# Performance work log

Measured on AMD Instinct MI355X. Metric: run time of the kernel, lower is better.

Reference implementation:

```python
import jax, jax.numpy as jnp
import numpy as np

HIDDEN = 1024
FFN = 2048
NUM_EXPERTS = 8
TOP_K = 2
BATCH, SEQ = 2, 1024


def setup_inputs() -> dict:
    key = jax.random.key(0)
    k0, k1, k2, k3, k4 = jax.random.split(key, 5)
    scale = 0.02
    hidden_states = jax.random.normal(k0, (BATCH, SEQ, HIDDEN), dtype=jnp.float32)
    gate_w = jax.random.normal(k1, (NUM_EXPERTS, HIDDEN), dtype=jnp.float32) * scale
    w1 = jax.random.normal(k2, (NUM_EXPERTS, FFN, HIDDEN), dtype=jnp.float32) * scale  # gate proj
    w3 = jax.random.normal(k3, (NUM_EXPERTS, FFN, HIDDEN), dtype=jnp.float32) * scale  # up proj
    w2 = jax.random.normal(k4, (NUM_EXPERTS, HIDDEN, FFN), dtype=jnp.float32) * scale  # down proj
    return {"hidden_states": hidden_states, "gate_w": gate_w, "w1": w1, "w2": w2, "w3": w3}


def reference(hidden_states, gate_w, w1, w2, w3):
    B, S, D = hidden_states.shape
    x = hidden_states.reshape(-1, D)                         # [T, D]
    T = x.shape[0]
    # Router: logits -> fp32 softmax -> top-k -> renormalize
    router_logits = jnp.einsum("td,ed->te", x, gate_w)       # [T, E]
    routing_weights = jax.nn.softmax(router_logits.astype(jnp.float32), axis=1)
    top_vals, top_idx = jax.lax.top_k(routing_weights, TOP_K)  # [T, K]
    top_vals = top_vals / jnp.sum(top_vals, axis=-1, keepdims=True)
    top_vals = top_vals.astype(x.dtype)
    # Per-token-per-expert combine weight (0 for unselected experts)
    w_te = jnp.zeros((T, NUM_EXPERTS), dtype=x.dtype)
    w_te = w_te.at[jnp.arange(T)[:, None], top_idx].add(top_vals)  # [T, E]
    # Fused experts: silu(x W1^T) * (x W3^T) -> W2^T, weighted combine
    g = jax.nn.silu(jnp.einsum("td,efd->tef", x, w1))        # [T, E, F]
    u = jnp.einsum("td,efd->tef", x, w3)                     # [T, E, F]
    y = jnp.einsum("tef,edf->ted", g * u, w2)                # [T, E, D]
    out = jnp.einsum("ted,te->td", y, w_te)                  # [T, D]
    return out.reshape(B, S, D), router_logits
```

## Files before the change

kernel.cpp:

```cpp
#include <hip/hip_runtime.h>
#include <hip/hip_bf16.h>
#include <stdint.h>

#define HIDDEN  1024
#define FFN_DIM 2048
#define NEXP    8
#define NTOK    2048
#define MAXROWS 5120

typedef short bf16x8 __attribute__((ext_vector_type(8)));
typedef float f32x4  __attribute__((ext_vector_type(4)));

static const size_t OFF_CNT  = 0;
static const size_t OFF_BASE = 64;
static const size_t OFF_TOK  = 128;
static const size_t OFF_WGT  = OFF_TOK + (size_t)NEXP*NTOK*4;
static const size_t OFF_XBF  = 131328;
static const size_t XBF_B    = (size_t)NTOK*HIDDEN*2;
static const size_t OFF_H    = OFF_XBF + XBF_B;
static const size_t H_B      = (size_t)MAXROWS*FFN_DIM*2;
static const size_t WS_NEED  = OFF_H + H_B;

__device__ __forceinline__ unsigned short f2bf(float f) {
  union { float f; unsigned u; } a; a.f = f;
  unsigned r = a.u + 0x7fff + ((a.u >> 16) & 1);
  return (unsigned short)(r >> 16);
}

__device__ __forceinline__ bf16x8 cvt8b(float4 a, float4 b) {
  union { uint4 u; bf16x8 v; } r;
  asm("v_cvt_pk_bf16_f32 %0, %1, %2" : "=v"(r.u.x) : "v"(a.x), "v"(a.y));
  asm("v_cvt_pk_bf16_f32 %0, %1, %2" : "=v"(r.u.y) : "v"(a.z), "v"(a.w));
  asm("v_cvt_pk_bf16_f32 %0, %1, %2" : "=v"(r.u.z) : "v"(b.x), "v"(b.y));
  asm("v_cvt_pk_bf16_f32 %0, %1, %2" : "=v"(r.u.w) : "v"(b.z), "v"(b.w));
  return r.v;
}

__device__ __forceinline__ void ld_g2l16(const void* gsrc, void* ldst) {
  __builtin_amdgcn_global_load_lds(
      (const __attribute__((address_space(1))) unsigned int*)gsrc,
      (__attribute__((address_space(3))) unsigned int*)ldst, 16, 0, 0);
}

__global__ __launch_bounds__(256) void router_kernel(
    const float* __restrict__ x, const float* __restrict__ gw,
    float* __restrict__ logits, int* __restrict__ cnt,
    int* __restrict__ tok, float* __restrict__ wgt,
    unsigned short* __restrict__ xbf)
{
  const int t   = blockIdx.x;
  const int tid = threadIdx.x;
  float4 xv = ((const float4*)(x + (size_t)t * HIDDEN))[tid];
  if (xbf) {
    ushort4 o;
    o.x = f2bf(xv.x); o.y = f2bf(xv.y); o.z = f2bf(xv.z); o.w = f2bf(xv.w);
    ((ushort4*)(xbf + (size_t)t * HIDDEN))[tid] = o;
  }
  float p[NEXP];
#pragma unroll
  for (int e = 0; e < NEXP; ++e) {
    float4 gv = ((const float4*)(gw + (size_t)e * HIDDEN))[tid];
    p[e] = xv.x * gv.x + xv.y * gv.y + xv.z * gv.z + xv.w * gv.w;
  }
#pragma unroll
  for (int e = 0; e < NEXP; ++e) {
#pragma unroll
    for (int off = 32; off > 0; off >>= 1)
      p[e] += __shfl_down(p[e], off, 64);
  }
  __shared__ float red[4][NEXP];
  const int wv = tid >> 6, ln = tid & 63;
  if (ln == 0) {
#pragma unroll
    for (int e = 0; e < NEXP; ++e) red[wv][e] = p[e];
  }
  __syncthreads();
  if (tid == 0) {
    float l[NEXP];
#pragma unroll
    for (int e = 0; e < NEXP; ++e) {
      l[e] = red[0][e] + red[1][e] + red[2][e] + red[3][e];
      logits[(size_t)t * NEXP + e] = l[e];
    }
    int i0 = 0;
#pragma unroll
    for (int e = 1; e < NEXP; ++e) if (l[e] > l[i0]) i0 = e;
    int i1 = (i0 == 0) ? 1 : 0;
#pragma unroll
    for (int e = 0; e < NEXP; ++e) if (e != i0 && l[e] > l[i1]) i1 = e;
    float w0 = 1.f / (1.f + expf(l[i1] - l[i0]));
    float w1 = 1.f - w0;
    int s0 = atomicAdd(&cnt[i0], 1);
    tok[i0 * NTOK + s0] = t;  wgt[i0 * NTOK + s0] = w0;
    int s1 = atomicAdd(&cnt[i1], 1);
    tok[i1 * NTOK + s1] = t;  wgt[i1 * NTOK + s1] = w1;
  }
}

__global__ void prefix_kernel(const int* __restrict__ cnt, int* __restrict__ base) {
  if (threadIdx.x == 0 && blockIdx.x == 0) {
    int b = 0;
#pragma unroll
    for (int e = 0; e < NEXP; ++e) { base[e] = b; b += ((cnt[e] + 127) >> 7) << 7; }
    base[NEXP] = b;
  }
}

__global__ __launch_bounds__(256, 3) void gemm1_kernel(
    const unsigned short* __restrict__ xbf,
    const float* __restrict__ w1f,
    const float* __restrict__ w3f,
    const int* __restrict__ cnt, const int* __restrict__ base,
    const int* __restrict__ tok,
    unsigned short* __restrict__ H)
{
  const int bid  = blockIdx.x;
  const int e    = bid & 7;
  const int slot = bid >> 3;
  const int mt   = slot & 15;
  const int nt   = slot >> 4;
  const int n = cnt[e];
  if (mt * 128 >= n) return;
  const int t = threadIdx.x;
  const int w = t >> 6, l = t & 63;

  __shared__ unsigned short Xs[128 * 64];
  __shared__ float W1s[64 * 64];
  __shared__ float W3s[64 * 64];

  const int xr   = t >> 3;
  const int xkey = ((t & 7) ^ (xr & 7)) << 3;
  const unsigned short* xp[4];
#pragma unroll
  for (int c = 0; c < 4; ++c) {
    int row = min(mt * 128 + c * 32 + xr, n - 1);
    xp[c] = xbf + (size_t)tok[e * NTOK + row] * HIDDEN + xkey;
  }

  const int wr   = t >> 4;
  const int wkey = ((t & 15) ^ wr) << 2;
  const float* w1p = w1f + (size_t)e * FFN_DIM * HIDDEN + ((size_t)nt * 64 + wr) * HIDDEN + wkey;
  const float* w3p = w3f + (size_t)e * FFN_DIM * HIDDEN + ((size_t)nt * 64 + wr) * HIDDEN + wkey;

  f32x4 acc1[4][2], acc3[4][2];
#pragma unroll
  for (int i = 0; i < 4; ++i)
#pragma unroll
    for (int j = 0; j < 2; ++j) { acc1[i][j] = (f32x4)0.f; acc3[i][j] = (f32x4)0.f; }

  const int Moff = (w & 1) * 64;
  const int Noff = (w >> 1) * 32;
  const int lr = l & 15;
  const int lg = l >> 4;

  for (int kb = 0; kb < HIDDEN / 64; ++kb) {
    __syncthreads();
    const int ko = kb * 64;
#pragma unroll
    for (int c = 0; c < 4; ++c)
      ld_g2l16(xp[c] + ko, (char*)Xs + c * 4096 + w * 1024);
#pragma unroll
    for (int c = 0; c < 4; ++c) {
      ld_g2l16(w1p + (size_t)c * 16 * HIDDEN + ko, (char*)W1s + c * 4096 + w * 1024);
      ld_g2l16(w3p + (size_t)c * 16 * HIDDEN + ko, (char*)W3s + c * 4096 + w * 1024);
    }
    __syncthreads();
#pragma unroll
    for (int s = 0; s < 2; ++s) {
      const int ub = 4 * s + lg;
      bf16x8 a[4];
#pragma unroll
      for (int mi = 0; mi < 4; ++mi) {
        const int R = Moff + mi * 16 + lr;
        a[mi] = *(const bf16x8*)((const char*)Xs + R * 128 + ((ub ^ (R & 7)) << 4));
      }
#pragma unroll
      for (int ni = 0; ni < 2; ++ni) {
        const int R  = Noff + ni * 16 + lr;
        const int p0 = (2 * ub) ^ (R & 15);
        float4 lo1 = *(const float4*)((const char*)W1s + R * 256 + (p0 << 4));
        float4 hi1 = *(const float4*)((const char*)W1s + R * 256 + ((p0 ^ 1) << 4));
        float4 lo3 = *(const float4*)((const char*)W3s + R * 256 + (p0 << 4));
        float4 hi3 = *(const float4*)((const char*)W3s + R * 256 + ((p0 ^ 1) << 4));
        bf16x8 b1 = cvt8b(lo1, hi1);
        bf16x8 b3 = cvt8b(lo3, hi3);
#pragma unroll
        for (int mi = 0; mi < 4; ++mi) {
          acc1[mi][ni] = __builtin_amdgcn_mfma_f32_16x16x32_bf16(a[mi], b1, acc1[mi][ni], 0, 0, 0);
          acc3[mi][ni] = __builtin_amdgcn_mfma_f32_16x16x32_bf16(a[mi], b3, acc3[mi][ni], 0, 0, 0);
        }
      }
    }
  }

  const size_t rbase = (size_t)base[e] + (size_t)mt * 128;
#pragma unroll
  for (int mi = 0; mi < 4; ++mi)
#pragma unroll
    for (int ni = 0; ni < 2; ++ni)
#pragma unroll
      for (int j = 0; j < 4; ++j) {
        int row = Moff + mi * 16 + lg * 4 + j;
        int col = nt * 64 + Noff + ni * 16 + lr;
        float s1 = acc1[mi][ni][j], s3 = acc3[mi][ni][j];
        float h = (s1 / (1.f + __expf(-s1))) * s3;
        H[(rbase + row) * FFN_DIM + col] = f2bf(h);
      }
}

__global__ __launch_bounds__(256, 4) void gemm2_kernel(
    const unsigned short* __restrict__ H,
    const float* __restrict__ w2f,
    const int* __restrict__ cnt, const int* __restrict__ base,
    const int* __restrict__ tok, const float* __restrict__ wgt,
    float* __restrict__ out)
{
  const int bid  = blockIdx.x;
  const int e    = bid & 7;
  const int slot = bid >> 3;
  const int mt   = slot & 15;
  const int nt   = (slot >> 4) & 15;
  const int sk   = slot >> 8;
  const int n = cnt[e];
  if (mt * 128 >= n) return;
  const int t = threadIdx.x;
  const int w = t >> 6, l = t & 63;

  __shared__ unsigned short Hs[128 * 64];
  __shared__ float W2s[64 * 64];
  __shared__ int   stok[128];
  __shared__ float swgt[128];

  if (t < 128) {
    int idx = mt * 128 + t;
    int ok = idx < n;
    stok[t] = ok ? tok[e * NTOK + idx] : -1;
    swgt[t] = ok ? wgt[e * NTOK + idx] : 0.f;
  }

  const int xr   = t >> 3;
  const int xkey = ((t & 7) ^ (xr & 7)) << 3;
  const unsigned short* Hp = H + (size_t)(base[e] + mt * 128 + xr) * FFN_DIM
                               + sk * (FFN_DIM / 2) + xkey;
  const int wr   = t >> 4;
  const int wkey = ((t & 15) ^ wr) << 2;
  const float* w2p = w2f + (size_t)e * HIDDEN * FFN_DIM + ((size_t)nt * 64 + wr) * FFN_DIM
                        + sk * (FFN_DIM / 2) + wkey;

  f32x4 acc[4][2];
#pragma unroll
  for (int i = 0; i < 4; ++i)
#pragma unroll
    for (int j = 0; j < 2; ++j) acc[i][j] = (f32x4)0.f;

  const int Moff = (w & 1) * 64;
  const int Noff = (w >> 1) * 32;
  const int lr = l & 15;
  const int lg = l >> 4;

  for (int kb = 0; kb < FFN_DIM / 2 / 64; ++kb) {
    __syncthreads();
    const int ko = kb * 64;
#pragma unroll
    for (int c = 0; c < 4; ++c)
      ld_g2l16(Hp + (size_t)c * 32 * FFN_DIM + ko, (char*)Hs + c * 4096 + w * 1024);
#pragma unroll
    for (int c = 0; c < 4; ++c)
      ld_g2l16(w2p + (size_t)c * 16 * FFN_DIM + ko, (char*)W2s + c * 4096 + w * 1024);
    __syncthreads();
#pragma unroll
    for (int s = 0; s < 2; ++s) {
      const int ub = 4 * s + lg;
      bf16x8 a[4];
#pragma unroll
      for (int mi = 0; mi < 4; ++mi) {
        const int R = Moff + mi * 16 + lr;
        a[mi] = *(const bf16x8*)((const char*)Hs + R * 128 + ((ub ^ (R & 7)) << 4));
      }
#pragma unroll
      for (int ni = 0; ni < 2; ++ni) {
        const int R  = Noff + ni * 16 + lr;
        const int p0 = (2 * ub) ^ (R & 15);
        float4 lo = *(const float4*)((const char*)W2s + R * 256 + (p0 << 4));
        float4 hi = *(const float4*)((const char*)W2s + R * 256 + ((p0 ^ 1) << 4));
        bf16x8 b = cvt8b(lo, hi);
#pragma unroll
        for (int mi = 0; mi < 4; ++mi)
          acc[mi][ni] = __builtin_amdgcn_mfma_f32_16x16x32_bf16(a[mi], b, acc[mi][ni], 0, 0, 0);
      }
    }
  }

#pragma unroll
  for (int mi = 0; mi < 4; ++mi)
#pragma unroll
    for (int ni = 0; ni < 2; ++ni)
#pragma unroll
      for (int j = 0; j < 4; ++j) {
        int row = Moff + mi * 16 + lg * 4 + j;
        int tk = stok[row];
        if (tk >= 0) {
          int col = nt * 64 + Noff + ni * 16 + lr;
          atomicAdd(&out[(size_t)tk * HIDDEN + col], swgt[row] * acc[mi][ni][j]);
        }
      }
}

#define TT 12
#define FC 256
#define NCHUNK (FFN_DIM / FC)

__global__ __launch_bounds__(256) void moe_ffn_kernel(
    const float* __restrict__ x,
    const float* __restrict__ w1, const float* __restrict__ w2,
    const float* __restrict__ w3,
    const int* __restrict__ cnt, const int* __restrict__ tok,
    const float* __restrict__ wgt, float* __restrict__ out)
{
  const int e  = blockIdx.y;
  const int n  = cnt[e];
  const int ts = blockIdx.x * TT;
  if (ts >= n) return;
  const int tid = threadIdx.x;

  __shared__ float xs[TT * HIDDEN];
  __shared__ float hc[TT * FC];
  __shared__ int   stok[TT];
  __shared__ float swgt[TT];

  if (tid < TT) {
    int idx = ts + tid;
    int tk  = (idx < n) ? tok[e * NTOK + idx] : -1;
    stok[tid] = tk;
    swgt[tid] = (idx < n) ? wgt[e * NTOK + idx] : 0.f;
  }
  __syncthreads();
#pragma unroll
  for (int i = 0; i < TT; ++i) {
    int tk = stok[i];
    float4 v = make_float4(0.f, 0.f, 0.f, 0.f);
    if (tk >= 0) v = ((const float4*)(x + (size_t)tk * HIDDEN))[tid];
    ((float4*)(xs + i * HIDDEN))[tid] = v;
  }
  __syncthreads();

  const float* w1e = w1 + (size_t)e * FFN_DIM * HIDDEN;
  const float* w3e = w3 + (size_t)e * FFN_DIM * HIDDEN;
  const float* w2e = w2 + (size_t)e * HIDDEN * FFN_DIM;

  float yacc[4][TT];
#pragma unroll
  for (int j = 0; j < 4; ++j)
#pragma unroll
    for (int t = 0; t < TT; ++t) yacc[j][t] = 0.f;

  for (int c = 0; c < NCHUNK; ++c) {
    const int f = c * FC + tid;
    const float4* r1 = (const float4*)(w1e + (size_t)f * HIDDEN);
    const float4* r3 = (const float4*)(w3e + (size_t)f * HIDDEN);
    float a1[TT], a3[TT];
#pragma unroll
    for (int t = 0; t < TT; ++t) { a1[t] = 0.f; a3[t] = 0.f; }
    for (int k = 0; k < HIDDEN / 4; ++k) {
      float4 v1 = r1[k];
      float4 v3 = r3[k];
#pragma unroll
      for (int t = 0; t < TT; ++t) {
        float4 xv = *(const float4*)(xs + t * HIDDEN + 4 * k);
        a1[t] += xv.x * v1.x + xv.y * v1.y + xv.z * v1.z + xv.w * v1.w;
        a3[t] += xv.x * v3.x + xv.y * v3.y + xv.z * v3.z + xv.w * v3.w;
      }
    }
    __syncthreads();
#pragma unroll
    for (int t = 0; t < TT; ++t) {
      float g  = a1[t];
      float sg = g / (1.f + __expf(-g));
      hc[t * FC + tid] = sg * a3[t];
    }
    __syncthreads();
    const float4* r20 = (const float4*)(w2e + (size_t)(tid      ) * FFN_DIM + c * FC);
    const float4* r21 = (const float4*)(w2e + (size_t)(tid + 256) * FFN_DIM + c * FC);
    const float4* r22 = (const float4*)(w2e + (size_t)(tid + 512) * FFN_DIM + c * FC);
    const float4* r23 = (const float4*)(w2e + (size_t)(tid + 768) * FFN_DIM + c * FC);
    for (int k = 0; k < FC / 4; ++k) {
      float4 wv0 = r20[k], wv1 = r21[k], wv2 = r22[k], wv3 = r23[k];
#pragma unroll
      for (int t = 0; t < TT; ++t) {
        float4 hv = *(const float4*)(hc + t * FC + 4 * k);
        yacc[0][t] += hv.x * wv0.x + hv.y * wv0.y + hv.z * wv0.z + hv.w * wv0.w;
        yacc[1][t] += hv.x * wv1.x + hv.y * wv1.y + hv.z * wv1.z + hv.w * wv1.w;
        yacc[2][t] += hv.x * wv2.x + hv.y * wv2.y + hv.z * wv2.z + hv.w * wv2.w;
        yacc[3][t] += hv.x * wv3.x + hv.y * wv3.y + hv.z * wv3.z + hv.w * wv3.w;
      }
    }
  }

#pragma unroll
  for (int t = 0; t < TT; ++t) {
    int tk = stok[t];
    if (tk < 0) continue;
    float wt = swgt[t];
    float* orow = out + (size_t)tk * HIDDEN;
    atomicAdd(orow + tid,       wt * yacc[0][t]);
    atomicAdd(orow + tid + 256, wt * yacc[1][t]);
    atomicAdd(orow + tid + 512, wt * yacc[2][t]);
    atomicAdd(orow + tid + 768, wt * yacc[3][t]);
  }
}

extern "C" void kernel_launch(void* const* d_in, const int* in_sizes, int n_in,
                              void* d_out, int out_size, void* d_ws, size_t ws_size,
                              hipStream_t stream) {
  const float* x  = (const float*)d_in[0];
  const float* gw = (const float*)d_in[1];
  const float* w1 = (const float*)d_in[2];
  const float* w2 = (const float*)d_in[3];
  const float* w3 = (const float*)d_in[4];
  float* out    = (float*)d_out;
  float* logits = out + (size_t)NTOK * HIDDEN;

  char* ws = (char*)d_ws;
  int*   cnt  = (int*)(ws + OFF_CNT);
  int*   base = (int*)(ws + OFF_BASE);
  int*   tokp = (int*)(ws + OFF_TOK);
  float* wgtp = (float*)(ws + OFF_WGT);

  const bool big = (ws_size >= WS_NEED);
  unsigned short* xbf  = big ? (unsigned short*)(ws + OFF_XBF) : (unsigned short*)0;
  unsigned short* Hbuf = big ? (unsigned short*)(ws + OFF_H)   : (unsigned short*)0;

  hipMemsetAsync(out, 0, (size_t)NTOK * HIDDEN * sizeof(float), stream);
  hipMemsetAsync(cnt, 0, NEXP * sizeof(int), stream);

  router_kernel<<<NTOK, 256, 0, stream>>>(x, gw, logits, cnt, tokp, wgtp, xbf);

  if (big) {
    prefix_kernel<<<1, 64, 0, stream>>>(cnt, base);
    gemm1_kernel<<<NEXP * 16 * 32, 256, 0, stream>>>(xbf, w1, w3, cnt, base, tokp, Hbuf);
    gemm2_kernel<<<NEXP * 16 * 16 * 2, 256, 0, stream>>>(Hbuf, w2, cnt, base, tokp, wgtp, out);
  } else {
    dim3 grid((NTOK + TT - 1) / TT, NEXP);
    moe_ffn_kernel<<<grid, 256, 0, stream>>>(x, w1, w2, w3, cnt, tokp, wgtp, out);
  }
}
```

Before: 196.8 us.

## Double-buffer weight tiles in expert GEMMs to prefetch next k-block

Both expert GEMM kernels now keep two LDS buffers for the fp32 weight tiles and issue the next k-block's weight loads before computing on the current one. Manual vmcnt waits and raw s_barrier calls replace the two __syncthreads per iteration, so the weight fetch for the next step overlaps the MFMA work. The larger LDS footprint lowers the launch-bounds occupancy hints (3 to 2 for gemm1, 4 to 3 for gemm2), trading resident waves for latency hiding. The hand-written waitcnt counts rely on exact load-instruction counts being correct.

Result: slower. 207.7 us (+5.6%).

```diff
diff --git a/kernel.cpp b/kernel.cpp
--- a/kernel.cpp
+++ b/kernel.cpp
@@ -106,7 +106,7 @@
   }
 }
 
-__global__ __launch_bounds__(256, 3) void gemm1_kernel(
+__global__ __launch_bounds__(256, 2) void gemm1_kernel(
     const unsigned short* __restrict__ xbf,
     const float* __restrict__ w1f,
     const float* __restrict__ w3f,
@@ -125,8 +125,8 @@
   const int w = t >> 6, l = t & 63;
 
   __shared__ unsigned short Xs[128 * 64];
-  __shared__ float W1s[64 * 64];
-  __shared__ float W3s[64 * 64];
+  __shared__ float W1s[2][64 * 64];
+  __shared__ float W3s[2][64 * 64];
 
   const int xr   = t >> 3;
   const int xkey = ((t & 7) ^ (xr & 7)) << 3;
@@ -153,18 +153,32 @@
   const int lr = l & 15;
   const int lg = l >> 4;
 
+#pragma unroll
+  for (int c = 0; c < 4; ++c) {
+    ld_g2l16(w1p + (size_t)c * 16 * HIDDEN, (char*)W1s[0] + c * 4096 + w * 1024);
+    ld_g2l16(w3p + (size_t)c * 16 * HIDDEN, (char*)W3s[0] + c * 4096 + w * 1024);
+  }
+
   for (int kb = 0; kb < HIDDEN / 64; ++kb) {
-    __syncthreads();
     const int ko = kb * 64;
+    const int cb = kb & 1, nb = cb ^ 1;
 #pragma unroll
     for (int c = 0; c < 4; ++c)
       ld_g2l16(xp[c] + ko, (char*)Xs + c * 4096 + w * 1024);
-#pragma unroll
-    for (int c = 0; c < 4; ++c) {
-      ld_g2l16(w1p + (size_t)c * 16 * HIDDEN + ko, (char*)W1s + c * 4096 + w * 1024);
-      ld_g2l16(w3p + (size_t)c * 16 * HIDDEN + ko, (char*)W3s + c * 4096 + w * 1024);
-    }
-    __syncthreads();
+    if (kb < HIDDEN / 64 - 1) {
+#pragma unroll
+      for (int c = 0; c < 4; ++c) {
+        ld_g2l16(w1p + (size_t)c * 16 * HIDDEN + ko + 64, (char*)W1s[nb] + c * 4096 + w * 1024);
+        ld_g2l16(w3p + (size_t)c * 16 * HIDDEN + ko + 64, (char*)W3s[nb] + c * 4096 + w * 1024);
+      }
+      __builtin_amdgcn_sched_barrier(0);
+      asm volatile("s_waitcnt vmcnt(8)" ::: "memory");
+    } else {
+      __builtin_amdgcn_sched_barrier(0);
+      asm volatile("s_waitcnt vmcnt(0)" ::: "memory");
+    }
+    __builtin_amdgcn_s_barrier();
+    __builtin_amdgcn_sched_barrier(0);
 #pragma unroll
     for (int s = 0; s < 2; ++s) {
       const int ub = 4 * s + lg;
@@ -178,10 +192,10 @@
       for (int ni = 0; ni < 2; ++ni) {
         const int R  = Noff + ni * 16 + lr;
         const int p0 = (2 * ub) ^ (R & 15);
-        float4 lo1 = *(const float4*)((const char*)W1s + R * 256 + (p0 << 4));
-        float4 hi1 = *(const float4*)((const char*)W1s + R * 256 + ((p0 ^ 1) << 4));
-        float4 lo3 = *(const float4*)((const char*)W3s + R * 256 + (p0 << 4));
-        float4 hi3 = *(const float4*)((const char*)W3s + R * 256 + ((p0 ^ 1) << 4));
+        float4 lo1 = *(const float4*)((const char*)W1s[cb] + R * 256 + (p0 << 4));
+        float4 hi1 = *(const float4*)((const char*)W1s[cb] + R * 256 + ((p0 ^ 1) << 4));
+        float4 lo3 = *(const float4*)((const char*)W3s[cb] + R * 256 + (p0 << 4));
+        float4 hi3 = *(const float4*)((const char*)W3s[cb] + R * 256 + ((p0 ^ 1) << 4));
         bf16x8 b1 = cvt8b(lo1, hi1);
         bf16x8 b3 = cvt8b(lo3, hi3);
 #pragma unroll
@@ -191,6 +205,9 @@
         }
       }
     }
+    __builtin_amdgcn_sched_barrier(0);
+    asm volatile("s_waitcnt lgkmcnt(0)" ::: "memory");
+    __builtin_amdgcn_s_barrier();
   }
 
   const size_t rbase = (size_t)base[e] + (size_t)mt * 128;
@@ -208,7 +225,7 @@
       }
 }
 
-__global__ __launch_bounds__(256, 4) void gemm2_kernel(
+__global__ __launch_bounds__(256, 3) void gemm2_kernel(
     const unsigned short* __restrict__ H,
     const float* __restrict__ w2f,
     const int* __restrict__ cnt, const int* __restrict__ base,
@@ -227,7 +244,7 @@
   const int w = t >> 6, l = t & 63;
 
   __shared__ unsigned short Hs[128 * 64];
-  __shared__ float W2s[64 * 64];
+  __shared__ float W2s[2][64 * 64];
   __shared__ int   stok[128];
   __shared__ float swgt[128];
 
@@ -258,16 +275,28 @@
   const int lr = l & 15;
   const int lg = l >> 4;
 
+#pragma unroll
+  for (int c = 0; c < 4; ++c)
+    ld_g2l16(w2p + (size_t)c * 16 * FFN_DIM, (char*)W2s[0] + c * 4096 + w * 1024);
+
   for (int kb = 0; kb < FFN_DIM / 2 / 64; ++kb) {
-    __syncthreads();
     const int ko = kb * 64;
+    const int cb = kb & 1, nb = cb ^ 1;
 #pragma unroll
     for (int c = 0; c < 4; ++c)
       ld_g2l16(Hp + (size_t)c * 32 * FFN_DIM + ko, (char*)Hs + c * 4096 + w * 1024);
-#pragma unroll
-    for (int c = 0; c < 4; ++c)
-      ld_g2l16(w2p + (size_t)c * 16 * FFN_DIM + ko, (char*)W2s + c * 4096 + w * 1024);
-    __syncthreads();
+    if (kb < FFN_DIM / 2 / 64 - 1) {
+#pragma unroll
+      for (int c = 0; c < 4; ++c)
+        ld_g2l16(w2p + (size_t)c * 16 * FFN_DIM + ko + 64, (char*)W2s[nb] + c * 4096 + w * 1024);
+      __builtin_amdgcn_sched_barrier(0);
+      asm volatile("s_waitcnt vmcnt(4)" ::: "memory");
+    } else {
+      __builtin_amdgcn_sched_barrier(0);
+      asm volatile("s_waitcnt vmcnt(0)" ::: "memory");
+    }
+    __builtin_amdgcn_s_barrier();
+    __builtin_amdgcn_sched_barrier(0);
 #pragma unroll
     for (int s = 0; s < 2; ++s) {
       const int ub = 4 * s + lg;
@@ -281,14 +310,17 @@
       for (int ni = 0; ni < 2; ++ni) {
         const int R  = Noff + ni * 16 + lr;
         const int p0 = (2 * ub) ^ (R & 15);
-        float4 lo = *(const float4*)((const char*)W2s + R * 256 + (p0 << 4));
-        float4 hi = *(const float4*)((const char*)W2s + R * 256 + ((p0 ^ 1) << 4));
+        float4 lo = *(const float4*)((const char*)W2s[cb] + R * 256 + (p0 << 4));
+        float4 hi = *(const float4*)((const char*)W2s[cb] + R * 256 + ((p0 ^ 1) << 4));
         bf16x8 b = cvt8b(lo, hi);
 #pragma unroll
         for (int mi = 0; mi < 4; ++mi)
           acc[mi][ni] = __builtin_amdgcn_mfma_f32_16x16x32_bf16(a[mi], b, acc[mi][ni], 0, 0, 0);
       }
     }
+    __builtin_amdgcn_sched_barrier(0);
+    asm volatile("s_waitcnt lgkmcnt(0)" ::: "memory");
+    __builtin_amdgcn_s_barrier();
   }
 
 #pragma unroll
```

## Pre-convert expert weights to bf16 and retile GEMMs to 512-thread blocks

Applied to the files above, without the earlier changes.

Adds a grid-stride kernel that converts w1, w3 and w2 from fp32 to bf16 into new workspace regions on every call. Both expert GEMMs then stream bf16 weight tiles straight into LDS, dropping the per-tile fp32 LDS reads and in-loop conversions. The GEMMs also move to 512-thread blocks with 8 waves, each wave owning a 32x32 output sub-tile instead of 64x32. The trade-off is an extra full pass over all weights each call (about 192MB read, 96MB written) and a much larger workspace requirement; if the workspace is too small, the code falls back to the slow path.

Result: slower. 265.1 us (+34.7%).

```diff
diff --git a/kernel.cpp b/kernel.cpp
--- a/kernel.cpp
+++ b/kernel.cpp
@@ -17,7 +17,11 @@
 static const size_t OFF_WGT  = OFF_TOK + (size_t)NEXP*NTOK*4;
 static const size_t OFF_XBF  = 131328;
 static const size_t XBF_B    = (size_t)NTOK*HIDDEN*2;
-static const size_t OFF_H    = OFF_XBF + XBF_B;
+static const size_t OFF_W1B  = OFF_XBF + XBF_B;
+static const size_t W_B      = (size_t)NEXP*FFN_DIM*HIDDEN*2;
+static const size_t OFF_W3B  = OFF_W1B + W_B;
+static const size_t OFF_W2B  = OFF_W3B + W_B;
+static const size_t OFF_H    = OFF_W2B + W_B;
 static const size_t H_B      = (size_t)MAXROWS*FFN_DIM*2;
 static const size_t WS_NEED  = OFF_H + H_B;
 
@@ -27,13 +31,13 @@
   return (unsigned short)(r >> 16);
 }
 
-__device__ __forceinline__ bf16x8 cvt8b(float4 a, float4 b) {
-  union { uint4 u; bf16x8 v; } r;
-  asm("v_cvt_pk_bf16_f32 %0, %1, %2" : "=v"(r.u.x) : "v"(a.x), "v"(a.y));
-  asm("v_cvt_pk_bf16_f32 %0, %1, %2" : "=v"(r.u.y) : "v"(a.z), "v"(a.w));
-  asm("v_cvt_pk_bf16_f32 %0, %1, %2" : "=v"(r.u.z) : "v"(b.x), "v"(b.y));
-  asm("v_cvt_pk_bf16_f32 %0, %1, %2" : "=v"(r.u.w) : "v"(b.z), "v"(b.w));
-  return r.v;
+__device__ __forceinline__ uint4 cvt8u(float4 a, float4 b) {
+  uint4 r;
+  asm("v_cvt_pk_bf16_f32 %0, %1, %2" : "=v"(r.x) : "v"(a.x), "v"(a.y));
+  asm("v_cvt_pk_bf16_f32 %0, %1, %2" : "=v"(r.y) : "v"(a.z), "v"(a.w));
+  asm("v_cvt_pk_bf16_f32 %0, %1, %2" : "=v"(r.z) : "v"(b.x), "v"(b.y));
+  asm("v_cvt_pk_bf16_f32 %0, %1, %2" : "=v"(r.w) : "v"(b.z), "v"(b.w));
+  return r;
 }
 
 __device__ __forceinline__ void ld_g2l16(const void* gsrc, void* ldst) {
@@ -106,10 +110,29 @@
   }
 }
 
-__global__ __launch_bounds__(256, 3) void gemm1_kernel(
+__global__ __launch_bounds__(256) void cvtw_kernel(
+    const float* __restrict__ s0, const float* __restrict__ s1, const float* __restrict__ s2,
+    unsigned short* __restrict__ d0, unsigned short* __restrict__ d1, unsigned short* __restrict__ d2,
+    int n8)
+{
+  const int start  = blockIdx.x * blockDim.x + threadIdx.x;
+  const int stride = gridDim.x * blockDim.x;
+#pragma unroll
+  for (int pass = 0; pass < 3; ++pass) {
+    const float* s = (pass == 0) ? s0 : (pass == 1) ? s1 : s2;
+    unsigned short* d = (pass == 0) ? d0 : (pass == 1) ? d1 : d2;
+    for (int i = start; i < n8; i += stride) {
+      float4 a = ((const float4*)s)[2 * i];
+      float4 b = ((const float4*)s)[2 * i + 1];
+      ((uint4*)d)[i] = cvt8u(a, b);
+    }
+  }
+}
+
+__global__ __launch_bounds__(512, 6) void gemm1_kernel(
     const unsigned short* __restrict__ xbf,
-    const float* __restrict__ w1f,
-    const float* __restrict__ w3f,
+    const unsigned short* __restrict__ w1bf,
+    const unsigned short* __restrict__ w3bf,
     const int* __restrict__ cnt, const int* __restrict__ base,
     const int* __restrict__ tok,
     unsigned short* __restrict__ H)
@@ -124,78 +147,64 @@
   const int t = threadIdx.x;
   const int w = t >> 6, l = t & 63;
 
-  __shared__ unsigned short Xs[128 * 64];
-  __shared__ float W1s[64 * 64];
-  __shared__ float W3s[64 * 64];
-
-  const int xr   = t >> 3;
-  const int xkey = ((t & 7) ^ (xr & 7)) << 3;
-  const unsigned short* xp[4];
-#pragma unroll
-  for (int c = 0; c < 4; ++c) {
-    int row = min(mt * 128 + c * 32 + xr, n - 1);
-    xp[c] = xbf + (size_t)tok[e * NTOK + row] * HIDDEN + xkey;
-  }
-
-  const int wr   = t >> 4;
-  const int wkey = ((t & 15) ^ wr) << 2;
-  const float* w1p = w1f + (size_t)e * FFN_DIM * HIDDEN + ((size_t)nt * 64 + wr) * HIDDEN + wkey;
-  const float* w3p = w3f + (size_t)e * FFN_DIM * HIDDEN + ((size_t)nt * 64 + wr) * HIDDEN + wkey;
-
-  f32x4 acc1[4][2], acc3[4][2];
-#pragma unroll
-  for (int i = 0; i < 4; ++i)
+  __shared__ unsigned short Xs [128 * 64];
+  __shared__ unsigned short W1s[64 * 64];
+  __shared__ unsigned short W3s[64 * 64];
+
+  const int sr   = t >> 3;
+  const int kp   = ((t & 7) ^ (sr & 7)) << 3;
+  const unsigned short* xp0 = xbf + (size_t)tok[e * NTOK + min(mt * 128 + sr, n - 1)]      * HIDDEN + kp;
+  const unsigned short* xp1 = xbf + (size_t)tok[e * NTOK + min(mt * 128 + 64 + sr, n - 1)] * HIDDEN + kp;
+  const unsigned short* w1p = w1bf + (size_t)e * FFN_DIM * HIDDEN + ((size_t)nt * 64 + sr) * HIDDEN + kp;
+  const unsigned short* w3p = w3bf + (size_t)e * FFN_DIM * HIDDEN + ((size_t)nt * 64 + sr) * HIDDEN + kp;
+
+  f32x4 acc1[2][2], acc3[2][2];
+#pragma unroll
+  for (int i = 0; i < 2; ++i)
 #pragma unroll
     for (int j = 0; j < 2; ++j) { acc1[i][j] = (f32x4)0.f; acc3[i][j] = (f32x4)0.f; }
 
-  const int Moff = (w & 1) * 64;
-  const int Noff = (w >> 1) * 32;
+  const int Moff = (w & 3) * 32;
+  const int Noff = (w >> 2) * 32;
   const int lr = l & 15;
   const int lg = l >> 4;
 
   for (int kb = 0; kb < HIDDEN / 64; ++kb) {
     __syncthreads();
     const int ko = kb * 64;
-#pragma unroll
-    for (int c = 0; c < 4; ++c)
-      ld_g2l16(xp[c] + ko, (char*)Xs + c * 4096 + w * 1024);
-#pragma unroll
-    for (int c = 0; c < 4; ++c) {
-      ld_g2l16(w1p + (size_t)c * 16 * HIDDEN + ko, (char*)W1s + c * 4096 + w * 1024);
-      ld_g2l16(w3p + (size_t)c * 16 * HIDDEN + ko, (char*)W3s + c * 4096 + w * 1024);
-    }
+    ld_g2l16(xp0 + ko, (char*)Xs + w * 1024);
+    ld_g2l16(xp1 + ko, (char*)Xs + 8192 + w * 1024);
+    ld_g2l16(w1p + ko, (char*)W1s + w * 1024);
+    ld_g2l16(w3p + ko, (char*)W3s + w * 1024);
     __syncthreads();
 #pragma unroll
     for (int s = 0; s < 2; ++s) {
       const int ub = 4 * s + lg;
-      bf16x8 a[4];
-#pragma unroll
-      for (int mi = 0; mi < 4; ++mi) {
+      bf16x8 a[2], b1[2], b3[2];
+#pragma unroll
+      for (int mi = 0; mi < 2; ++mi) {
         const int R = Moff + mi * 16 + lr;
         a[mi] = *(const bf16x8*)((const char*)Xs + R * 128 + ((ub ^ (R & 7)) << 4));
       }
 #pragma unroll
       for (int ni = 0; ni < 2; ++ni) {
-        const int R  = Noff + ni * 16 + lr;
-        const int p0 = (2 * ub) ^ (R & 15);
-        float4 lo1 = *(const float4*)((const char*)W1s + R * 256 + (p0 << 4));
-        float4 hi1 = *(const float4*)((const char*)W1s + R * 256 + ((p0 ^ 1) << 4));
-        float4 lo3 = *(const float4*)((const char*)W3s + R * 256 + (p0 << 4));
-        float4 hi3 = *(const float4*)((const char*)W3s + R * 256 + ((p0 ^ 1) << 4));
-        bf16x8 b1 = cvt8b(lo1, hi1);
-        bf16x8 b3 = cvt8b(lo3, hi3);
-#pragma unroll
-        for (int mi = 0; mi < 4; ++mi) {
-          acc1[mi][ni] = __builtin_amdgcn_mfma_f32_16x16x32_bf16(a[mi], b1, acc1[mi][ni], 0, 0, 0);
-          acc3[mi][ni] = __builtin_amdgcn_mfma_f32_16x16x32_bf16(a[mi], b3, acc3[mi][ni], 0, 0, 0);
+        const int R = Noff + ni * 16 + lr;
+        b1[ni] = *(const bf16x8*)((const char*)W1s + R * 128 + ((ub ^ (R & 7)) << 4));
+        b3[ni] = *(const bf16x8*)((const char*)W3s + R * 128 + ((ub ^ (R & 7)) << 4));
+      }
+#pragma unroll
+      for (int mi = 0; mi < 2; ++mi)
+#pragma unroll
+        for (int ni = 0; ni < 2; ++ni) {
+          acc1[mi][ni] = __builtin_amdgcn_mfma_f32_16x16x32_bf16(a[mi], b1[ni], acc1[mi][ni], 0, 0, 0);
+          acc3[mi][ni] = __builtin_amdgcn_mfma_f32_16x16x32_bf16(a[mi], b3[ni], acc3[mi][ni], 0, 0, 0);
         }
-      }
     }
   }
 
   const size_t rbase = (size_t)base[e] + (size_t)mt * 128;
 #pragma unroll
-  for (int mi = 0; mi < 4; ++mi)
+  for (int mi = 0; mi < 2; ++mi)
 #pragma unroll
     for (int ni = 0; ni < 2; ++ni)
 #pragma unroll
@@ -208,9 +217,9 @@
       }
 }
 
-__global__ __launch_bounds__(256, 4) void gemm2_kernel(
+__global__ __launch_bounds__(512, 6) void gemm2_kernel(
     const unsigned short* __restrict__ H,
-    const float* __restrict__ w2f,
+    const unsigned short* __restrict__ w2bf,
     const int* __restrict__ cnt, const int* __restrict__ base,
     const int* __restrict__ tok, const float* __restrict__ wgt,
     float* __restrict__ out)
@@ -226,8 +235,8 @@
   const int t = threadIdx.x;
   const int w = t >> 6, l = t & 63;
 
-  __shared__ unsigned short Hs[128 * 64];
-  __shared__ float W2s[64 * 64];
+  __shared__ unsigned short Hs [128 * 64];
+  __shared__ unsigned short W2s[64 * 64];
   __shared__ int   stok[128];
   __shared__ float swgt[128];
 
@@ -238,61 +247,55 @@
     swgt[t] = ok ? wgt[e * NTOK + idx] : 0.f;
   }
 
-  const int xr   = t >> 3;
-  const int xkey = ((t & 7) ^ (xr & 7)) << 3;
-  const unsigned short* Hp = H + (size_t)(base[e] + mt * 128 + xr) * FFN_DIM
-                               + sk * (FFN_DIM / 2) + xkey;
-  const int wr   = t >> 4;
-  const int wkey = ((t & 15) ^ wr) << 2;
-  const float* w2p = w2f + (size_t)e * HIDDEN * FFN_DIM + ((size_t)nt * 64 + wr) * FFN_DIM
-                        + sk * (FFN_DIM / 2) + wkey;
-
-  f32x4 acc[4][2];
-#pragma unroll
-  for (int i = 0; i < 4; ++i)
+  const int sr = t >> 3;
+  const int kp = ((t & 7) ^ (sr & 7)) << 3;
+  const unsigned short* hp0 = H + (size_t)(base[e] + mt * 128 + sr)      * FFN_DIM + sk * (FFN_DIM / 2) + kp;
+  const unsigned short* hp1 = H + (size_t)(base[e] + mt * 128 + 64 + sr) * FFN_DIM + sk * (FFN_DIM / 2) + kp;
+  const unsigned short* w2p = w2bf + (size_t)e * HIDDEN * FFN_DIM + ((size_t)nt * 64 + sr) * FFN_DIM
+                                  + sk * (FFN_DIM / 2) + kp;
+
+  f32x4 acc[2][2];
+#pragma unroll
+  for (int i = 0; i < 2; ++i)
 #pragma unroll
     for (int j = 0; j < 2; ++j) acc[i][j] = (f32x4)0.f;
 
-  const int Moff = (w & 1) * 64;
-  const int Noff = (w >> 1) * 32;
+  const int Moff = (w & 3) * 32;
+  const int Noff = (w >> 2) * 32;
   const int lr = l & 15;
   const int lg = l >> 4;
 
   for (int kb = 0; kb < FFN_DIM / 2 / 64; ++kb) {
     __syncthreads();
     const int ko = kb * 64;
-#pragma unroll
-    for (int c = 0; c < 4; ++c)
-      ld_g2l16(Hp + (size_t)c * 32 * FFN_DIM + ko, (char*)Hs + c * 4096 + w * 1024);
-#pragma unroll
-    for (int c = 0; c < 4; ++c)
-      ld_g2l16(w2p + (size_t)c * 16 * FFN_DIM + ko, (char*)W2s + c * 4096 + w * 1024);
+    ld_g2l16(hp0 + ko, (char*)Hs + w * 1024);
+    ld_g2l16(hp1 + ko, (char*)Hs + 8192 + w * 1024);
+    ld_g2l16(w2p + ko, (char*)W2s + w * 1024);
     __syncthreads();
 #pragma unroll
     for (int s = 0; s < 2; ++s) {
       const int ub = 4 * s + lg;
-      bf16x8 a[4];
-#pragma unroll
-      for (int mi = 0; mi < 4; ++mi) {
+      bf16x8 a[2], b[2];
+#pragma unroll
+      for (int mi = 0; mi < 2; ++mi) {
         const int R = Moff + mi * 16 + lr;
         a[mi] = *(const bf16x8*)((const char*)Hs + R * 128 + ((ub ^ (R & 7)) << 4));
       }
 #pragma unroll
       for (int ni = 0; ni < 2; ++ni) {
-        const int R  = Noff + ni * 16 + lr;
-        const int p0 = (2 * ub) ^ (R & 15);
-        float4 lo = *(const float4*)((const char*)W2s + R * 256 + (p0 << 4));
-        float4 hi = *(const float4*)((const char*)W2s + R * 256 + ((p0 ^ 1) << 4));
-        bf16x8 b = cvt8b(lo, hi);
-#pragma unroll
-        for (int mi = 0; mi < 4; ++mi)
-          acc[mi][ni] = __builtin_amdgcn_mfma_f32_16x16x32_bf16(a[mi], b, acc[mi][ni], 0, 0, 0);
-      }
-    }
-  }
-
-#pragma unroll
-  for (int mi = 0; mi < 4; ++mi)
+        const int R = Noff + ni * 16 + lr;
+        b[ni] = *(const bf16x8*)((const char*)W2s + R * 128 + ((ub ^ (R & 7)) << 4));
+      }
+#pragma unroll
+      for (int mi = 0; mi < 2; ++mi)
+#pragma unroll
+        for (int ni = 0; ni < 2; ++ni)
+          acc[mi][ni] = __builtin_amdgcn_mfma_f32_16x16x32_bf16(a[mi], b[ni], acc[mi][ni], 0, 0, 0);
+    }
+  }
+
+#pragma unroll
+  for (int mi = 0; mi < 2; ++mi)
 #pragma unroll
     for (int ni = 0; ni < 2; ++ni)
 #pragma unroll
@@ -428,6 +431,9 @@
 
   const bool big = (ws_size >= WS_NEED);
   unsigned short* xbf  = big ? (unsigned short*)(ws + OFF_XBF) : (unsigned short*)0;
+  unsigned short* w1b  = big ? (unsigned short*)(ws + OFF_W1B) : (unsigned short*)0;
+  unsigned short* w3b  = big ? (unsigned short*)(ws + OFF_W3B) : (unsigned short*)0;
+  unsigned short* w2b  = big ? (unsigned short*)(ws + OFF_W2B) : (unsigned short*)0;
   unsigned short* Hbuf = big ? (unsigned short*)(ws + OFF_H)   : (unsigned short*)0;
 
   hipMemsetAsync(out, 0, (size_t)NTOK * HIDDEN * sizeof(float), stream);
@@ -436,9 +442,12 @@
   router_kernel<<<NTOK, 256, 0, stream>>>(x, gw, logits, cnt, tokp, wgtp, xbf);
 
   if (big) {
+    cvtw_kernel<<<2048, 256, 0, stream>>>(w1, w3, w2, w1b, w3b, w2b,
+                                          (int)((size_t)NEXP * FFN_DIM * HIDDEN / 8));
     prefix_kernel<<<1, 64, 0, stream>>>(cnt, base);
-    gemm1_kernel<<<NEXP * 16 * 32, 256, 0, stream>>>(xbf, w1, w3, cnt, base, tokp, Hbuf);
-    gemm2_kernel<<<NEXP * 16 * 16 * 2, 256, 0, stream>>>(Hbuf, w2, cnt, base, tokp, wgtp, out);
+
+    gemm1_kernel<<<NEXP * 16 * 32, 512, 0, stream>>>(xbf, w1b, w3b, cnt, base, tokp, Hbuf);
+    gemm2_kernel<<<NEXP * 16 * 16 * 2, 512, 0, stream>>>(Hbuf, w2b, cnt, base, tokp, wgtp, out);
   } else {
     dim3 grid((NTOK + TT - 1) / TT, NEXP);
     moe_ffn_kernel<<<grid, 256, 0, stream>>>(x, w1, w2, w3, cnt, tokp, wgtp, out);
```

## Halve M tile, double-buffer activations in LDS, load fp32 weights directly to registers

Applied to the files above, without the earlier changes.

Both expert GEMM kernels drop the M tile from 128 to 64 rows, with prefix padding and grid sizes changed to match. The activation tile is now double-buffered in LDS, so the next K block loads while the current one computes. The fp32 weight operands no longer go through LDS; each lane reads its B fragment straight from global memory into registers and converts it to bf16 there. This removes LDS traffic and one barrier per iteration and adds blocks for better occupancy. In exchange, weight bytes are re-read more often across M tiles, and global load latency is exposed inside the loop.

Result: slower. 604.8 us (+207.4%).

```diff
diff --git a/kernel.cpp b/kernel.cpp
--- a/kernel.cpp
+++ b/kernel.cpp
@@ -101,7 +101,7 @@
   if (threadIdx.x == 0 && blockIdx.x == 0) {
     int b = 0;
 #pragma unroll
-    for (int e = 0; e < NEXP; ++e) { base[e] = b; b += ((cnt[e] + 127) >> 7) << 7; }
+    for (int e = 0; e < NEXP; ++e) { base[e] = b; b += ((cnt[e] + 63) >> 6) << 6; }
     base[NEXP] = b;
   }
 }
@@ -117,85 +117,91 @@
   const int bid  = blockIdx.x;
   const int e    = bid & 7;
   const int slot = bid >> 3;
-  const int mt   = slot & 15;
-  const int nt   = slot >> 4;
+  const int mt   = slot & 31;
+  const int nt   = slot >> 5;
   const int n = cnt[e];
-  if (mt * 128 >= n) return;
+  if (mt * 64 >= n) return;
   const int t = threadIdx.x;
   const int w = t >> 6, l = t & 63;
 
-  __shared__ unsigned short Xs[128 * 64];
-  __shared__ float W1s[64 * 64];
-  __shared__ float W3s[64 * 64];
-
-  const int xr   = t >> 3;
-  const int xkey = ((t & 7) ^ (xr & 7)) << 3;
-  const unsigned short* xp[4];
-#pragma unroll
-  for (int c = 0; c < 4; ++c) {
-    int row = min(mt * 128 + c * 32 + xr, n - 1);
-    xp[c] = xbf + (size_t)tok[e * NTOK + row] * HIDDEN + xkey;
-  }
-
-  const int wr   = t >> 4;
-  const int wkey = ((t & 15) ^ wr) << 2;
-  const float* w1p = w1f + (size_t)e * FFN_DIM * HIDDEN + ((size_t)nt * 64 + wr) * HIDDEN + wkey;
-  const float* w3p = w3f + (size_t)e * FFN_DIM * HIDDEN + ((size_t)nt * 64 + wr) * HIDDEN + wkey;
-
-  f32x4 acc1[4][2], acc3[4][2];
-#pragma unroll
-  for (int i = 0; i < 4; ++i)
-#pragma unroll
-    for (int j = 0; j < 2; ++j) { acc1[i][j] = (f32x4)0.f; acc3[i][j] = (f32x4)0.f; }
-
-  const int Moff = (w & 1) * 64;
+  __shared__ unsigned short Xs[2][64 * 64];
+
+  const int lrow = (t >> 3) & 7;
+  const int kp   = ((t & 7) ^ lrow) << 3;
+  const int row0 = (w * 2    ) * 8 + lrow;
+  const int row1 = (w * 2 + 1) * 8 + lrow;
+  const unsigned short* xq0 = xbf + (size_t)tok[e * NTOK + min(mt * 64 + row0, n - 1)] * HIDDEN + kp;
+  const unsigned short* xq1 = xbf + (size_t)tok[e * NTOK + min(mt * 64 + row1, n - 1)] * HIDDEN + kp;
+
+  const int Moff = (w & 1) * 32;
   const int Noff = (w >> 1) * 32;
   const int lr = l & 15;
   const int lg = l >> 4;
 
+  const size_t eoff = (size_t)e * FFN_DIM * HIDDEN;
+  const float* b1p[2];
+  const float* b3p[2];
+#pragma unroll
+  for (int ni = 0; ni < 2; ++ni) {
+    const size_t rg = (size_t)(nt * 64 + Noff + ni * 16 + lr);
+    b1p[ni] = w1f + eoff + rg * HIDDEN + lg * 8;
+    b3p[ni] = w3f + eoff + rg * HIDDEN + lg * 8;
+  }
+
+  f32x4 acc1[2][2], acc3[2][2];
+#pragma unroll
+  for (int i = 0; i < 2; ++i)
+#pragma unroll
+    for (int j = 0; j < 2; ++j) { acc1[i][j] = (f32x4)0.f; acc3[i][j] = (f32x4)0.f; }
+
+  ld_g2l16(xq0, (char*)Xs[0] + (w * 2    ) * 1024);
+  ld_g2l16(xq1, (char*)Xs[0] + (w * 2 + 1) * 1024);
+  __syncthreads();
+
   for (int kb = 0; kb < HIDDEN / 64; ++kb) {
-    __syncthreads();
+    const int cur = kb & 1;
+    if (kb + 1 < HIDDEN / 64) {
+      ld_g2l16(xq0 + (kb + 1) * 64, (char*)Xs[cur ^ 1] + (w * 2    ) * 1024);
+      ld_g2l16(xq1 + (kb + 1) * 64, (char*)Xs[cur ^ 1] + (w * 2 + 1) * 1024);
+    }
     const int ko = kb * 64;
-#pragma unroll
-    for (int c = 0; c < 4; ++c)
-      ld_g2l16(xp[c] + ko, (char*)Xs + c * 4096 + w * 1024);
-#pragma unroll
-    for (int c = 0; c < 4; ++c) {
-      ld_g2l16(w1p + (size_t)c * 16 * HIDDEN + ko, (char*)W1s + c * 4096 + w * 1024);
-      ld_g2l16(w3p + (size_t)c * 16 * HIDDEN + ko, (char*)W3s + c * 4096 + w * 1024);
-    }
-    __syncthreads();
+    float4 lo[2][2][2], hi[2][2][2];
+#pragma unroll
+    for (int ni = 0; ni < 2; ++ni)
+#pragma unroll
+      for (int s = 0; s < 2; ++s) {
+        lo[0][ni][s] = *(const float4*)(b1p[ni] + ko + 32 * s);
+        hi[0][ni][s] = *(const float4*)(b1p[ni] + ko + 32 * s + 4);
+        lo[1][ni][s] = *(const float4*)(b3p[ni] + ko + 32 * s);
+        hi[1][ni][s] = *(const float4*)(b3p[ni] + ko + 32 * s + 4);
+      }
+    const char* Xc = (const char*)Xs[cur];
 #pragma unroll
     for (int s = 0; s < 2; ++s) {
       const int ub = 4 * s + lg;
-      bf16x8 a[4];
-#pragma unroll
-      for (int mi = 0; mi < 4; ++mi) {
+      bf16x8 a[2];
+#pragma unroll
+      for (int mi = 0; mi < 2; ++mi) {
         const int R = Moff + mi * 16 + lr;
-        a[mi] = *(const bf16x8*)((const char*)Xs + R * 128 + ((ub ^ (R & 7)) << 4));
+        a[mi] = *(const bf16x8*)(Xc + R * 128 + ((ub ^ (R & 7)) << 4));
       }
 #pragma unroll
       for (int ni = 0; ni < 2; ++ni) {
-        const int R  = Noff + ni * 16 + lr;
-        const int p0 = (2 * ub) ^ (R & 15);
-        float4 lo1 = *(const float4*)((const char*)W1s + R * 256 + (p0 << 4));
-        float4 hi1 = *(const float4*)((const char*)W1s + R * 256 + ((p0 ^ 1) << 4));
-        float4 lo3 = *(const float4*)((const char*)W3s + R * 256 + (p0 << 4));
-        float4 hi3 = *(const float4*)((const char*)W3s + R * 256 + ((p0 ^ 1) << 4));
-        bf16x8 b1 = cvt8b(lo1, hi1);
-        bf16x8 b3 = cvt8b(lo3, hi3);
-#pragma unroll
-        for (int mi = 0; mi < 4; ++mi) {
+        bf16x8 b1 = cvt8b(lo[0][ni][s], hi[0][ni][s]);
+        bf16x8 b3 = cvt8b(lo[1][ni][s], hi[1][ni][s]);
+#pragma unroll
+        for (int mi = 0; mi < 2; ++mi) {
           acc1[mi][ni] = __builtin_amdgcn_mfma_f32_16x16x32_bf16(a[mi], b1, acc1[mi][ni], 0, 0, 0);
           acc3[mi][ni] = __builtin_amdgcn_mfma_f32_16x16x32_bf16(a[mi], b3, acc3[mi][ni], 0, 0, 0);
         }
       }
     }
-  }
-
-  const size_t rbase = (size_t)base[e] + (size_t)mt * 128;
-#pragma unroll
-  for (int mi = 0; mi < 4; ++mi)
+    __syncthreads();
+  }
+
+  const size_t rbase = (size_t)base[e] + (size_t)mt * 64;
+#pragma unroll
+  for (int mi = 0; mi < 2; ++mi)
 #pragma unroll
     for (int ni = 0; ni < 2; ++ni)
 #pragma unroll
@@ -218,81 +224,93 @@
   const int bid  = blockIdx.x;
   const int e    = bid & 7;
   const int slot = bid >> 3;
-  const int mt   = slot & 15;
-  const int nt   = (slot >> 4) & 15;
-  const int sk   = slot >> 8;
+  const int mt   = slot & 31;
+  const int nt   = (slot >> 5) & 15;
+  const int sk   = slot >> 9;
   const int n = cnt[e];
-  if (mt * 128 >= n) return;
+  if (mt * 64 >= n) return;
   const int t = threadIdx.x;
   const int w = t >> 6, l = t & 63;
 
-  __shared__ unsigned short Hs[128 * 64];
-  __shared__ float W2s[64 * 64];
-  __shared__ int   stok[128];
-  __shared__ float swgt[128];
-
-  if (t < 128) {
-    int idx = mt * 128 + t;
+  __shared__ unsigned short Hs[2][64 * 64];
+  __shared__ int   stok[64];
+  __shared__ float swgt[64];
+
+  if (t < 64) {
+    int idx = mt * 64 + t;
     int ok = idx < n;
     stok[t] = ok ? tok[e * NTOK + idx] : -1;
     swgt[t] = ok ? wgt[e * NTOK + idx] : 0.f;
   }
 
-  const int xr   = t >> 3;
-  const int xkey = ((t & 7) ^ (xr & 7)) << 3;
-  const unsigned short* Hp = H + (size_t)(base[e] + mt * 128 + xr) * FFN_DIM
-                               + sk * (FFN_DIM / 2) + xkey;
-  const int wr   = t >> 4;
-  const int wkey = ((t & 15) ^ wr) << 2;
-  const float* w2p = w2f + (size_t)e * HIDDEN * FFN_DIM + ((size_t)nt * 64 + wr) * FFN_DIM
-                        + sk * (FFN_DIM / 2) + wkey;
-
-  f32x4 acc[4][2];
-#pragma unroll
-  for (int i = 0; i < 4; ++i)
-#pragma unroll
-    for (int j = 0; j < 2; ++j) acc[i][j] = (f32x4)0.f;
-
-  const int Moff = (w & 1) * 64;
+  const int lrow = (t >> 3) & 7;
+  const int kp   = ((t & 7) ^ lrow) << 3;
+  const int row0 = (w * 2    ) * 8 + lrow;
+  const int row1 = (w * 2 + 1) * 8 + lrow;
+  const unsigned short* hq0 = H + (size_t)(base[e] + mt * 64 + row0) * FFN_DIM + sk * (FFN_DIM / 2) + kp;
+  const unsigned short* hq1 = H + (size_t)(base[e] + mt * 64 + row1) * FFN_DIM + sk * (FFN_DIM / 2) + kp;
+
+  const int Moff = (w & 1) * 32;
   const int Noff = (w >> 1) * 32;
   const int lr = l & 15;
   const int lg = l >> 4;
 
-  for (int kb = 0; kb < FFN_DIM / 2 / 64; ++kb) {
-    __syncthreads();
+  const float* b2p[2];
+#pragma unroll
+  for (int ni = 0; ni < 2; ++ni) {
+    const size_t rg = (size_t)(nt * 64 + Noff + ni * 16 + lr);
+    b2p[ni] = w2f + (size_t)e * HIDDEN * FFN_DIM + rg * FFN_DIM + sk * (FFN_DIM / 2) + lg * 8;
+  }
+
+  f32x4 acc[2][2];
+#pragma unroll
+  for (int i = 0; i < 2; ++i)
+#pragma unroll
+    for (int j = 0; j < 2; ++j) acc[i][j] = (f32x4)0.f;
+
+  ld_g2l16(hq0, (char*)Hs[0] + (w * 2    ) * 1024);
+  ld_g2l16(hq1, (char*)Hs[0] + (w * 2 + 1) * 1024);
+  __syncthreads();
+
+  const int NK = FFN_DIM / 2 / 64;
+  for (int kb = 0; kb < NK; ++kb) {
+    const int cur = kb & 1;
+    if (kb + 1 < NK) {
+      ld_g2l16(hq0 + (kb + 1) * 64, (char*)Hs[cur ^ 1] + (w * 2    ) * 1024);
+      ld_g2l16(hq1 + (kb + 1) * 64, (char*)Hs[cur ^ 1] + (w * 2 + 1) * 1024);
+    }
     const int ko = kb * 64;
-#pragma unroll
-    for (int c = 0; c < 4; ++c)
-      ld_g2l16(Hp + (size_t)c * 32 * FFN_DIM + ko, (char*)Hs + c * 4096 + w * 1024);
-#pragma unroll
-    for (int c = 0; c < 4; ++c)
-      ld_g2l16(w2p + (size_t)c * 16 * FFN_DIM + ko, (char*)W2s + c * 4096 + w * 1024);
-    __syncthreads();
+    float4 lo[2][2], hi[2][2];
+#pragma unroll
+    for (int ni = 0; ni < 2; ++ni)
+#pragma unroll
+      for (int s = 0; s < 2; ++s) {
+        lo[ni][s] = *(const float4*)(b2p[ni] + ko + 32 * s);
+        hi[ni][s] = *(const float4*)(b2p[ni] + ko + 32 * s + 4);
+      }
+    const char* Hc = (const char*)Hs[cur];
 #pragma unroll
     for (int s = 0; s < 2; ++s) {
       const int ub = 4 * s + lg;
-      bf16x8 a[4];
-#pragma unroll
-      for (int mi = 0; mi < 4; ++mi) {
+      bf16x8 a[2];
+#pragma unroll
+      for (int mi = 0; mi < 2; ++mi) {
         const int R = Moff + mi * 16 + lr;
-        a[mi] = *(const bf16x8*)((const char*)Hs + R * 128 + ((ub ^ (R & 7)) << 4));
+        a[mi] = *(const bf16x8*)(Hc + R * 128 + ((ub ^ (R & 7)) << 4));
       }
 #pragma unroll
       for (int ni = 0; ni < 2; ++ni) {
-        const int R  = Noff + ni * 16 + lr;
-        const int p0 = (2 * ub) ^ (R & 15);
-        float4 lo = *(const float4*)((const char*)W2s + R * 256 + (p0 << 4));
-        float4 hi = *(const float4*)((const char*)W2s + R * 256 + ((p0 ^ 1) << 4));
-        bf16x8 b = cvt8b(lo, hi);
-#pragma unroll
-        for (int mi = 0; mi < 4; ++mi)
+        bf16x8 b = cvt8b(lo[ni][s], hi[ni][s]);
+#pragma unroll
+        for (int mi = 0; mi < 2; ++mi)
           acc[mi][ni] = __builtin_amdgcn_mfma_f32_16x16x32_bf16(a[mi], b, acc[mi][ni], 0, 0, 0);
       }
     }
-  }
-
-#pragma unroll
-  for (int mi = 0; mi < 4; ++mi)
+    __syncthreads();
+  }
+
+#pragma unroll
+  for (int mi = 0; mi < 2; ++mi)
 #pragma unroll
     for (int ni = 0; ni < 2; ++ni)
 #pragma unroll
@@ -437,8 +455,8 @@
 
   if (big) {
     prefix_kernel<<<1, 64, 0, stream>>>(cnt, base);
-    gemm1_kernel<<<NEXP * 16 * 32, 256, 0, stream>>>(xbf, w1, w3, cnt, base, tokp, Hbuf);
-    gemm2_kernel<<<NEXP * 16 * 16 * 2, 256, 0, stream>>>(Hbuf, w2, cnt, base, tokp, wgtp, out);
+    gemm1_kernel<<<NEXP * 32 * 32, 256, 0, stream>>>(xbf, w1, w3, cnt, base, tokp, Hbuf);
+    gemm2_kernel<<<NEXP * 32 * 16 * 2, 256, 0, stream>>>(Hbuf, w2, cnt, base, tokp, wgtp, out);
   } else {
     dim3 grid((NTOK + TT - 1) / TT, NEXP);
     moe_ffn_kernel<<<grid, 256, 0, stream>>>(x, w1, w2, w3, cnt, tokp, wgtp, out);
```
